# Kernel tuning notes

Measured on AMD Instinct MI355X. Metric: run time of the kernel, lower is better.

## Reference

```python
import jax, jax.numpy as jnp
import numpy as np
import math

B, SEQ_LEN, ENC_IN = 8, 1021, 12
D_MODEL, N_HEADS, D_FF, E_LAYERS = 512, 8, 2048, 3
FACTOR, NUM_CLASS = 5, 10
BN_EPS = 1e-5


def _pos_encoding(L, d):
    pos = np.arange(L, dtype=np.float32)[:, None]
    div = np.exp(np.arange(0, d, 2, dtype=np.float32) * (-math.log(10000.0) / d))
    pe = np.zeros((L, d), dtype=np.float32)
    pe[:, 0::2] = np.sin(pos * div)
    pe[:, 1::2] = np.cos(pos * div)
    return jnp.asarray(pe)


def _layer_norm(x, w, b, eps=1e-5):
    mu = jnp.mean(x, -1, keepdims=True)
    var = jnp.mean((x - mu) ** 2, -1, keepdims=True)
    return (x - mu) * jax.lax.rsqrt(var + eps) * w + b


def _circ_conv1d(x, w, b=None):
    # x: [B,C,L], w: [O,C,3]; circular pad 1 each side then valid conv (torch padding_mode='circular')
    xp = jnp.concatenate([x[..., -1:], x, x[..., :1]], axis=-1)
    y = jax.lax.conv_general_dilated(xp, w, (1,), 'VALID', dimension_numbers=('NCH', 'OIH', 'NCH'))
    return y if b is None else y + b[None, :, None]


def _prob_attention(q, k, v, rng):
    # ProbSparse attention (mask_flag=False). q,k,v: [B,H,L,Dh]
    Bq, H, L, Dh = q.shape
    n = min(FACTOR * int(math.ceil(math.log(L))), L)      # U_part == u (L_Q == L_K)
    idx = jax.random.randint(rng, (L, n), 0, L)           # sampled key ids per query
    k_sample = k[:, :, idx, :]                            # [B,H,L,n,Dh]
    qk_sample = jnp.einsum('bhld,bhlsd->bhls', q, k_sample)
    m = qk_sample.max(-1) - qk_sample.sum(-1) / L         # sparsity measure M
    _, m_top = jax.lax.top_k(m, n)                        # [B,H,n] active queries
    q_red = jnp.take_along_axis(q, m_top[..., None], axis=2)   # [B,H,n,Dh]
    scores = jnp.einsum('bhud,bhld->bhul', q_red, k) * (1.0 / math.sqrt(Dh))
    attn = jax.nn.softmax(scores, axis=-1)
    upd = jnp.einsum('bhul,bhld->bhud', attn, v)          # [B,H,n,Dh]
    ctx = jnp.broadcast_to(jnp.mean(v, axis=2, keepdims=True), (Bq, H, L, Dh))  # initial context = mean(V)
    b_ix = jnp.arange(Bq)[:, None, None]
    h_ix = jnp.arange(H)[None, :, None]
    ctx = ctx.at[b_ix, h_ix, m_top].set(upd)
    return jnp.transpose(ctx, (0, 2, 1, 3))               # [B,L,H,Dh]


def _encoder_layer(x, l, attn_wq, attn_bq, attn_wk, attn_bk, attn_wv, attn_bv,
                   attn_wo, attn_bo, ln1_w, ln1_b, ln2_w, ln2_b,
                   ff1_w, ff1_b, ff2_w, ff2_b, rng):
    Bx, L, dm = x.shape
    Dh = dm // N_HEADS
    q = (x @ attn_wq[l].T + attn_bq[l]).reshape(Bx, L, N_HEADS, Dh).transpose(0, 2, 1, 3)
    k = (x @ attn_wk[l].T + attn_bk[l]).reshape(Bx, L, N_HEADS, Dh).transpose(0, 2, 1, 3)
    v = (x @ attn_wv[l].T + attn_bv[l]).reshape(Bx, L, N_HEADS, Dh).transpose(0, 2, 1, 3)
    ctx = _prob_attention(q, k, v, rng).reshape(Bx, L, dm)
    new_x = ctx @ attn_wo[l].T + attn_bo[l]
    x = _layer_norm(x + new_x, ln1_w[l], ln1_b[l])
    y = jax.nn.gelu(x @ ff1_w[l].T + ff1_b[l], approximate=False)
    y = y @ ff2_w[l].T + ff2_b[l]
    return _layer_norm(x + y, ln2_w[l], ln2_b[l])


def _conv_layer(x, cw, cb, bnw, bnb):
    # distillation: circular conv -> BatchNorm (eval, mean 0 / var 1) -> ELU -> MaxPool(3,2,pad=1)
    h = _circ_conv1d(jnp.transpose(x, (0, 2, 1)), cw, cb)
    h = h * (bnw * (1.0 / math.sqrt(1.0 + BN_EPS)))[None, :, None] + bnb[None, :, None]
    h = jax.nn.elu(h)
    h = jax.lax.reduce_window(h, -np.inf, jax.lax.max, (1, 1, 3), (1, 1, 2),
                              ((0, 0), (0, 0), (1, 1)))
    return jnp.transpose(h, (0, 2, 1))


def _forward(x_enc, tok_w, attn_wq, attn_bq, attn_wk, attn_bk, attn_wv, attn_bv,
             attn_wo, attn_bo, ln1_w, ln1_b, ln2_w, ln2_b, ff1_w, ff1_b, ff2_w, ff2_b,
             cv_w, cv_b, bn_w, bn_b, norm_w, norm_b, proj_w, proj_b):
    rngs = jax.random.split(jax.random.key(42), E_LAYERS)
    # DataEmbedding = TokenEmbedding (circular conv, no bias) + sinusoidal positional
    x = jnp.transpose(_circ_conv1d(jnp.transpose(x_enc, (0, 2, 1)), tok_w), (0, 2, 1))
    x = x + _pos_encoding(x.shape[1], D_MODEL)[None]
    for l in range(E_LAYERS):
        x = _encoder_layer(x, l, attn_wq, attn_bq, attn_wk, attn_bk, attn_wv, attn_bv,
                           attn_wo, attn_bo, ln1_w, ln1_b, ln2_w, ln2_b,
                           ff1_w, ff1_b, ff2_w, ff2_b, rngs[l])
        if l < E_LAYERS - 1:
            x = _conv_layer(x, cv_w[l], cv_b[l], bn_w[l], bn_b[l])
    x = _layer_norm(x, norm_w, norm_b)
    out = jax.nn.gelu(x, approximate=False)
    out = out.reshape(out.shape[0], -1)    # [B, d_model * conv_seq_len]
    return out @ proj_w.T + proj_b


def setup_inputs() -> dict:
    key = jax.random.key(0)
    ks = jax.random.split(key, 32)
    d, ff = D_MODEL, D_FF

    def nrm(k, shape, scale=1.0):
        return jax.random.normal(k, shape, dtype=jnp.float32) * scale

    s_d = 1.0 / math.sqrt(d)
    return {
        'x_enc': nrm(ks[0], (B, SEQ_LEN, ENC_IN)),
        'tok_w': nrm(ks[1], (d, ENC_IN, 3), 1.0 / math.sqrt(ENC_IN * 3)),
        'attn_wq': nrm(ks[2], (E_LAYERS, d, d), s_d), 'attn_bq': nrm(ks[3], (E_LAYERS, d), 0.02),
        'attn_wk': nrm(ks[4], (E_LAYERS, d, d), s_d), 'attn_bk': nrm(ks[5], (E_LAYERS, d), 0.02),
        'attn_wv': nrm(ks[6], (E_LAYERS, d, d), s_d), 'attn_bv': nrm(ks[7], (E_LAYERS, d), 0.02),
        'attn_wo': nrm(ks[8], (E_LAYERS, d, d), s_d), 'attn_bo': nrm(ks[9], (E_LAYERS, d), 0.02),
        'ln1_w': jnp.ones((E_LAYERS, d), jnp.float32), 'ln1_b': jnp.zeros((E_LAYERS, d), jnp.float32),
        'ln2_w': jnp.ones((E_LAYERS, d), jnp.float32), 'ln2_b': jnp.zeros((E_LAYERS, d), jnp.float32),
        'ff1_w': nrm(ks[10], (E_LAYERS, ff, d), s_d), 'ff1_b': nrm(ks[11], (E_LAYERS, ff), 0.02),
        'ff2_w': nrm(ks[12], (E_LAYERS, d, ff), 1.0 / math.sqrt(ff)), 'ff2_b': nrm(ks[13], (E_LAYERS, d), 0.02),
        'cv_w': nrm(ks[14], (E_LAYERS - 1, d, d, 3), 1.0 / math.sqrt(3 * d)),
        'cv_b': nrm(ks[15], (E_LAYERS - 1, d), 0.02),
        'bn_w': jnp.ones((E_LAYERS - 1, d), jnp.float32), 'bn_b': jnp.zeros((E_LAYERS - 1, d), jnp.float32),
        'norm_w': jnp.ones((d,), jnp.float32), 'norm_b': jnp.zeros((d,), jnp.float32),
        'proj_w': nrm(ks[16], (NUM_CLASS, d * 256), 1.0 / math.sqrt(d * 256)),
        'proj_b': jnp.zeros((NUM_CLASS,), jnp.float32),
    }


def reference(x_enc, tok_w, attn_wq, attn_bq, attn_wk, attn_bk, attn_wv, attn_bv,
              attn_wo, attn_bo, ln1_w, ln1_b, ln2_w, ln2_b, ff1_w, ff1_b, ff2_w, ff2_b,
              cv_w, cv_b, bn_w, bn_b, norm_w, norm_b, proj_w, proj_b):
    return _forward(x_enc, tok_w, attn_wq, attn_bq, attn_wk, attn_bk, attn_wv, attn_bv,
                    attn_wo, attn_bo, ln1_w, ln1_b, ln2_w, ln2_b, ff1_w, ff1_b, ff2_w, ff2_b,
                    cv_w, cv_b, bn_w, bn_b, norm_w, norm_b, proj_w, proj_b)
```

## Files before the change

### kernel.cpp

```cpp
#include <hip/hip_runtime.h>
#include <math.h>
#include <stdint.h>

typedef __attribute__((ext_vector_type(8))) short bf16x8;
typedef __attribute__((ext_vector_type(4))) float f32x4;

__device__ __forceinline__ unsigned short f2bf(float f){
  unsigned int u = __float_as_uint(f);
  unsigned int r = (u + 0x7fffu + ((u>>16)&1u)) >> 16;
  return (unsigned short)r;
}
__device__ __forceinline__ float bf2f(unsigned short h){
  return __uint_as_float(((unsigned int)h)<<16);
}
__device__ __forceinline__ void gload16(const void* g, void* l){
  __builtin_amdgcn_global_load_lds(
      (const __attribute__((address_space(1))) unsigned int*)g,
      (__attribute__((address_space(3))) unsigned int*)l, 16, 0, 0);
}

__host__ __device__ static inline uint32_t rotl32(uint32_t x, int d){ return (x<<d)|(x>>(32-d)); }
__host__ __device__ static inline void tf2x32(uint32_t k0, uint32_t k1, uint32_t c0, uint32_t c1,
                                              uint32_t* o0, uint32_t* o1){
  uint32_t ks0=k0, ks1=k1, ks2=k0^k1^0x1BD11BDAu;
  uint32_t x0=c0+ks0, x1=c1+ks1;
  const int ra[4]={13,15,26,6}, rb[4]={17,29,16,24};
  #pragma unroll
  for(int i=0;i<4;i++){x0+=x1;x1=rotl32(x1,ra[i]);x1^=x0;}
  x0+=ks1; x1+=ks2+1u;
  #pragma unroll
  for(int i=0;i<4;i++){x0+=x1;x1=rotl32(x1,rb[i]);x1^=x0;}
  x0+=ks2; x1+=ks0+2u;
  #pragma unroll
  for(int i=0;i<4;i++){x0+=x1;x1=rotl32(x1,ra[i]);x1^=x0;}
  x0+=ks0; x1+=ks1+3u;
  #pragma unroll
  for(int i=0;i<4;i++){x0+=x1;x1=rotl32(x1,rb[i]);x1^=x0;}
  x0+=ks1; x1+=ks2+4u;
  #pragma unroll
  for(int i=0;i<4;i++){x0+=x1;x1=rotl32(x1,ra[i]);x1^=x0;}
  x0+=ks2; x1+=ks0+5u;
  *o0=x0; *o1=x1;
}

__global__ __launch_bounds__(256) void gen_idx_k(uint32_t k1a,uint32_t k1b,
                                                 uint32_t k2a,uint32_t k2b,
                                                 int size,uint32_t span,uint32_t mult,
                                                 int* __restrict__ idx){
  int i = blockIdx.x*256 + threadIdx.x;
  if (i >= size) return;
  uint32_t h0,h1,l0,l1;
  tf2x32(k1a,k1b,0u,(uint32_t)i,&h0,&h1);
  tf2x32(k2a,k2b,0u,(uint32_t)i,&l0,&l1);
  uint32_t hb = h0^h1, lb = l0^l1;
  idx[i] = (int)((((hb%span)*mult) + (lb%span)) % span);
}

__global__ __launch_bounds__(256) void embed_k(const float* __restrict__ xe,
                                               const float* __restrict__ tw,
                                               float* __restrict__ X,
                                               short* __restrict__ Xh){
  int i = blockIdx.x*256 + threadIdx.x;
  int c = i & 511;
  int bl = i >> 9;
  int l = bl % 1021;
  int b = bl / 1021;
  float acc = 0.f;
  #pragma unroll
  for (int t=0;t<3;t++){
    int ls = l - 1 + t;
    ls = (ls < 0) ? 1020 : (ls >= 1021 ? 0 : ls);
    const float* xp = xe + (size_t)(b*1021 + ls)*12;
    const float* wp = tw + (size_t)c*36 + t;
    #pragma unroll
    for (int ci=0; ci<12; ci++) acc += xp[ci] * wp[ci*3];
  }
  int ip = c >> 1;
  float div = expf((float)(2*ip) * (float)(-9.210340371976184/512.0));
  float ang = (float)l * div;
  acc += (c & 1) ? cosf(ang) : sinf(ang);
  X[i] = acc;
  Xh[i] = f2bf(acc);
}

__global__ __launch_bounds__(256) void wcvt_k(const float* __restrict__ src,
                                              short* __restrict__ dst, int n){
  int i = blockIdx.x*256 + threadIdx.x;
  if (i < n) dst[i] = f2bf(src[i]);
}
__global__ __launch_bounds__(256) void convw_k(const float* __restrict__ cw,
                                               short* __restrict__ W){
  int i = blockIdx.x*256 + threadIdx.x;
  int col = i % 1536; int co = i / 1536;
  int t = col / 512; int ci = col % 512;
  W[i] = f2bf(cw[(size_t)co*1536 + ci*3 + t]);
}

__global__ __launch_bounds__(256) void gemm_bf16_k(
    const short* __restrict__ A, long Ab,
    const short* __restrict__ W, long Wb,
    const float* __restrict__ bias,
    float* __restrict__ Cf, short* __restrict__ Ch, long Cb,
    int M, int Nreal, int Nstride, int K, int mode,
    const float* __restrict__ s2, const float* __restrict__ b2,
    const float* __restrict__ rs, long rsb,
    short* __restrict__ KhG, int Lq)
{
  __shared__ short As[8192];
  __shared__ short Bs[8192];
  const int t = threadIdx.x;
  const int lane = t & 63;
  const int w = t >> 6;
  const int wr = w >> 1, wc = w & 1;
  const int z = blockIdx.z;
  const int m0 = blockIdx.x * 128, n0 = blockIdx.y * 128;
  const short* Az = A + (size_t)z * Ab;
  const short* Wz = W + (size_t)z * Wb;

  f32x4 acc[4][4];
  #pragma unroll
  for (int i=0;i<4;i++)
    #pragma unroll
    for (int j=0;j<4;j++) acc[i][j] = (f32x4){0.f,0.f,0.f,0.f};

  const int r0  = t >> 2;
  const int k80 = (t & 3) << 3;
  char* AsB = (char*)As;
  char* BsB = (char*)Bs;

  #define STAGE(buf, k0) do { \
    gload16(Az + (size_t)(m0 + r0)      * K + (k0) + k80, AsB + (buf)*8192 + (size_t)w*1024); \
    gload16(Az + (size_t)(m0 + r0 + 64) * K + (k0) + k80, AsB + (buf)*8192 + 4096 + (size_t)w*1024); \
    gload16(Wz + (size_t)(n0 + r0)      * K + (k0) + k80, BsB + (buf)*8192 + (size_t)w*1024); \
    gload16(Wz + (size_t)(n0 + r0 + 64) * K + (k0) + k80, BsB + (buf)*8192 + 4096 + (size_t)w*1024); \
  } while(0)

  STAGE(0, 0);
  __syncthreads();
  int cur = 0;
  for (int k0 = 0; k0 < K; k0 += 32){
    if (k0 + 32 < K) STAGE(cur^1, k0+32);
    bf16x8 a[4], b[4];
    #pragma unroll
    for (int mi=0; mi<4; mi++){
      int aoff = cur*4096 + (wr*64 + mi*16 + (lane&15))*32 + ((lane>>4)<<3);
      a[mi] = *(const bf16x8*)(&As[aoff]);
    }
    #pragma unroll
    for (int ni=0; ni<4; ni++){
      int boff = cur*4096 + (wc*64 + ni*16 + (lane&15))*32 + ((lane>>4)<<3);
      b[ni] = *(const bf16x8*)(&Bs[boff]);
    }
    #pragma unroll
    for (int mi=0; mi<4; mi++)
      #pragma unroll
      for (int ni=0; ni<4; ni++)
        acc[mi][ni] = __builtin_amdgcn_mfma_f32_16x16x32_bf16(a[mi], b[ni], acc[mi][ni], 0, 0, 0);
    __syncthreads();
    cur ^= 1;
  }
  #undef STAGE

  #pragma unroll
  for (int mi=0; mi<4; mi++){
    #pragma unroll
    for (int r=0; r<4; r++){
      int gm = m0 + wr*64 + mi*16 + ((lane>>4)<<2) + r;
      if (gm >= M) continue;
      float rsc = (mode==4) ? rs[(size_t)z*rsb + gm] : 0.f;
      int bb = 0, ll = 0;
      if (KhG){ bb = gm / Lq; ll = gm - bb*Lq; }
      #pragma unroll
      for (int ni=0; ni<4; ni++){
        int gn = n0 + wc*64 + ni*16 + (lane&15);
        if (gn >= Nreal) continue;
        float v = acc[mi][ni][r];
        if (mode <= 2) v += bias[gn];
        if (mode == 1){
          v = 0.5f*v*(1.0f + erff(v*0.707106781186547524f));
        } else if (mode == 2){
          v = v * (s2[gn]*0.9999950000374997f) + b2[gn];
          v = (v > 0.f) ? v : expm1f(v);
        } else if (mode == 4){
          v *= rsc;
        }
        size_t off = (size_t)z*Cb + (size_t)gm*Nstride + gn;
        if (Cf) Cf[off] = v;
        if (Ch) Ch[off] = f2bf(v);
        if (KhG) KhG[(((size_t)bb*8 + (gn>>6))*1024 + ll)*64 + (gn&63)] = f2bf(v);
      }
    }
  }
}

__global__ __launch_bounds__(320) void qk_dot_k(const float* __restrict__ Q,
                                                const float* __restrict__ Kb,
                                                const int* __restrict__ idx,
                                                float* __restrict__ QK, int L, int n){
  __shared__ float Qs[512];
  int blk = blockIdx.x;
  int l = blk % L, b = blk / L;
  int t = threadIdx.x;
  if (t < 128){
    gload16(Q + (size_t)(b*L + l)*512 + t*4, (char*)Qs + (size_t)(t>>6)*1024);
  }
  __syncthreads();
  if (t < 8*n){
    int h = t / n, s = t - h*n;
    int kr = idx[l*n + s];
    const float4* kp = (const float4*)(Kb + (size_t)(b*L + kr)*512 + h*64);
    const float4* qp = (const float4*)(Qs + h*64);
    float dot = 0.f;
    #pragma unroll
    for (int i=0;i<16;i++){
      float4 a = qp[i], c = kp[i];
      dot += a.x*c.x + a.y*c.y + a.z*c.z + a.w*c.w;
    }
    QK[((size_t)(b*8 + h)*L + l)*n + s] = dot;
  }
}

__global__ __launch_bounds__(256) void reduce_m_k(const float* __restrict__ QK,
                                                  float* __restrict__ Mout, int L, int n){
  int gi = blockIdx.x*256 + threadIdx.x;
  if (gi >= 64*L) return;
  int l = gi % L; int bh = gi / L;
  const float* row = QK + (size_t)gi*n;
  float mx = -INFINITY, sm = 0.f;
  for (int s=0;s<n;s++){ float v = row[s]; mx = fmaxf(mx, v); sm += v; }
  Mout[(size_t)bh*1024 + l] = mx - sm/(float)L;
}

__global__ __launch_bounds__(64) void topk_k(const float* __restrict__ Mv,
                                             int* __restrict__ topk, int L, int n){
  int bh = blockIdx.x; int lane = threadIdx.x;
  float v[16];
  #pragma unroll
  for (int i=0;i<16;i++){ int l = i*64 + lane; v[i] = (l<L) ? Mv[(size_t)bh*1024 + l] : -INFINITY; }
  for (int it=0; it<n; ++it){
    float bv = -INFINITY; int bi = 0x7fffffff;
    #pragma unroll
    for (int i=0;i<16;i++){ int l = i*64+lane; if (v[i] > bv){ bv = v[i]; bi = l; } }
    #pragma unroll
    for (int o=32;o>0;o>>=1){
      float ov = __shfl_xor(bv, o); int oi = __shfl_xor(bi, o);
      if (ov > bv || (ov == bv && oi < bi)){ bv = ov; bi = oi; }
    }
    if (lane == 0) topk[bh*n + it] = bi;
    int wl = bi & 63, wi = bi >> 6;
    if (lane == wl){
      #pragma unroll
      for (int i=0;i<16;i++) if (i == wi) v[i] = -INFINITY;
    }
  }
}

__global__ __launch_bounds__(64) void qred_k(const float* __restrict__ Q,
                                             const int* __restrict__ topk,
                                             short* __restrict__ Qrh, int L, int n){
  int u = blockIdx.x % n; int bh = blockIdx.x / n;
  int h = bh & 7, b = bh >> 3; int d = threadIdx.x;
  int lq = topk[bh*n + u];
  Qrh[(size_t)bh*8192 + u*64 + d] = f2bf(0.125f * Q[(size_t)(b*L + lq)*512 + h*64 + d]);
}

__global__ __launch_bounds__(256) void vt_k(const float* __restrict__ V,
                                            short* __restrict__ Vt, int L){
  __shared__ float ts[64][65];
  int z = blockIdx.x >> 4;
  int l0 = (blockIdx.x & 15) * 64;
  int h = z & 7, b = z >> 3;
  int t = threadIdx.x;
  for (int i = t; i < 4096; i += 256){
    int lloc = i >> 6, d = i & 63;
    int l = l0 + lloc;
    ts[d][lloc] = (l < L) ? V[(size_t)(b*L + l)*512 + h*64 + d] : 0.f;
  }
  __syncthreads();
  for (int i = t; i < 4096; i += 256){
    int d = i >> 6, lloc = i & 63;
    Vt[(size_t)z*131072 + (size_t)d*1024 + l0 + lloc] = f2bf(ts[d][lloc]);
  }
}

__global__ __launch_bounds__(256) void softmax_k(const float* __restrict__ S,
                                                 short* __restrict__ Ph,
                                                 float* __restrict__ RS, int L, int n){
  int u = blockIdx.x % n; int z = blockIdx.x / n;
  const float* srow = S + (size_t)z*n*1024 + (size_t)u*1024;
  short* prow = Ph + (size_t)z*131072 + (size_t)u*1024;
  int t = threadIdx.x;
  __shared__ float red[256];
  float lm = -INFINITY;
  for (int l=t; l<L; l+=256) lm = fmaxf(lm, srow[l]);
  red[t]=lm; __syncthreads();
  for (int o=128;o>0;o>>=1){ if(t<o) red[t]=fmaxf(red[t],red[t+o]); __syncthreads(); }
  float mx = red[0]; __syncthreads();
  float ls = 0.f;
  for (int l=t; l<1024; l+=256){
    float p = (l < L) ? expf(srow[l]-mx) : 0.f;
    prow[l] = f2bf(p);
    ls += p;
  }
  red[t]=ls; __syncthreads();
  for (int o=128;o>0;o>>=1){ if(t<o) red[t]+=red[t+o]; __syncthreads(); }
  if (t==0) RS[(size_t)z*n + u] = 1.0f/red[0];
}

__global__ __launch_bounds__(512) void vmean_part_k(const float* __restrict__ V,
                                                    float* __restrict__ part, int L){
  int b = blockIdx.x; int j = blockIdx.y; int c = threadIdx.x;
  float s = 0.f;
  for (int l = j; l < L; l += 16) s += V[(size_t)(b*L + l)*512 + c];
  part[(size_t)(b*16 + j)*512 + c] = s;
}
__global__ __launch_bounds__(256) void vmean_comb_k(const float* __restrict__ part,
                                                    float* __restrict__ vmean, int L){
  int i = blockIdx.x*256 + threadIdx.x;
  int b = i >> 9; int c = i & 511;
  float s = 0.f;
  #pragma unroll
  for (int j=0;j<16;j++) s += part[(size_t)(b*16 + j)*512 + c];
  vmean[i] = s / (float)L;
}
__global__ __launch_bounds__(256) void ctx_fill_k(short* __restrict__ CTXh,
                                                  const float* __restrict__ vmean, int L){
  int i = blockIdx.x*256 + threadIdx.x;
  int c = i & 511; int bl = i >> 9; int b = bl / L;
  CTXh[i] = f2bf(vmean[b*512 + c]);
}
__global__ __launch_bounds__(256) void ctx_scatter_k(short* __restrict__ CTXh,
                                                     const float* __restrict__ UPD,
                                                     const int* __restrict__ topk, int L, int n){
  int i = blockIdx.x*256 + threadIdx.x;
  int d = i & 63; int u = (i >> 6) % n; int bh = i / (64*n);
  int h = bh & 7; int b = bh >> 3;
  int lq = topk[bh*n + u];
  CTXh[(size_t)(b*L + lq)*512 + h*64 + d] = f2bf(UPD[((size_t)bh*n + u)*64 + d]);
}

__global__ __launch_bounds__(256) void add_ln_k(float* __restrict__ X,
                                                short* __restrict__ Xh,
                                                const float* __restrict__ Y,
                                                const float* __restrict__ w,
                                                const float* __restrict__ b){
  int r = blockIdx.x;
  size_t base = (size_t)r*512;
  int t = threadIdx.x;
  float v0 = X[base+t]     + Y[base+t];
  float v1 = X[base+t+256] + Y[base+t+256];
  __shared__ float red[256];
  red[t] = v0 + v1; __syncthreads();
  for (int o=128;o>0;o>>=1){ if(t<o) red[t]+=red[t+o]; __syncthreads(); }
  float mu = red[0]*(1.f/512.f); __syncthreads();
  float d0 = v0-mu, d1 = v1-mu;
  red[t] = d0*d0 + d1*d1; __syncthreads();
  for (int o=128;o>0;o>>=1){ if(t<o) red[t]+=red[t+o]; __syncthreads(); }
  float rs = 1.0f/sqrtf(red[0]*(1.f/512.f) + 1e-5f);
  float x0 = d0*rs*w[t]     + b[t];
  float x1 = d1*rs*w[t+256] + b[t+256];
  X[base+t]     = x0;  Xh[base+t]     = f2bf(x0);
  X[base+t+256] = x1;  Xh[base+t+256] = f2bf(x1);
}

__global__ __launch_bounds__(256) void ln_gelu_k(const float* __restrict__ X,
                                                 float* __restrict__ Yout,
                                                 const float* __restrict__ w,
                                                 const float* __restrict__ b){
  int r = blockIdx.x;
  size_t base = (size_t)r*512;
  int t = threadIdx.x;
  float v0 = X[base+t];
  float v1 = X[base+t+256];
  __shared__ float red[256];
  red[t] = v0 + v1; __syncthreads();
  for (int o=128;o>0;o>>=1){ if(t<o) red[t]+=red[t+o]; __syncthreads(); }
  float mu = red[0]*(1.f/512.f); __syncthreads();
  float d0 = v0-mu, d1 = v1-mu;
  red[t] = d0*d0 + d1*d1; __syncthreads();
  for (int o=128;o>0;o>>=1){ if(t<o) red[t]+=red[t+o]; __syncthreads(); }
  float rs = 1.0f/sqrtf(red[0]*(1.f/512.f) + 1e-5f);
  float g0 = d0*rs*w[t]     + b[t];
  float g1 = d1*rs*w[t+256] + b[t+256];
  Yout[base+t]     = 0.5f*g0*(1.0f + erff(g0*0.707106781186547524f));
  Yout[base+t+256] = 0.5f*g1*(1.0f + erff(g1*0.707106781186547524f));
}

__global__ __launch_bounds__(256) void im2col_k(const float* __restrict__ X,
                                                short* __restrict__ O, int L){
  int i = blockIdx.x*256 + threadIdx.x;
  int col = i % 1536; int bl = i / 1536;
  int l = bl % L; int b = bl / L;
  int t = col / 512; int ci = col % 512;
  int ls = l - 1 + t;
  ls = (ls < 0) ? (L-1) : (ls >= L ? 0 : ls);
  O[(size_t)bl*1536 + col] = f2bf(X[(size_t)(b*L + ls)*512 + ci]);
}
__global__ __launch_bounds__(256) void pool_k(const short* __restrict__ Hc,
                                              float* __restrict__ X,
                                              short* __restrict__ Xh, int L, int Lo){
  int i = blockIdx.x*256 + threadIdx.x;
  int c = i & 511; int r = i >> 9; int lo = r % Lo; int b = r / Lo;
  float m = -INFINITY;
  #pragma unroll
  for (int dt=-1; dt<=1; dt++){
    int li = 2*lo + dt;
    if (li >= 0 && li < L) m = fmaxf(m, bf2f((unsigned short)Hc[(size_t)(b*L + li)*512 + c]));
  }
  size_t o = (size_t)(b*Lo + lo)*512 + c;
  X[o] = m; Xh[o] = f2bf(m);
}

__global__ __launch_bounds__(256) void proj_part_k(const float* __restrict__ Xg,
                                                   const float* __restrict__ pw,
                                                   float* __restrict__ part){
  int b = blockIdx.x >> 5;
  int c = blockIdx.x & 31;
  int t = threadIdx.x;
  const float4* xp = (const float4*)(Xg + (size_t)b*131072 + (size_t)c*4096);
  float4 x0 = xp[t], x1 = xp[t+256], x2 = xp[t+512], x3 = xp[t+768];
  float acc[10];
  #pragma unroll
  for (int j=0;j<10;j++){
    const float4* wp = (const float4*)(pw + (size_t)j*131072 + (size_t)c*4096);
    float4 w0 = wp[t], w1 = wp[t+256], w2 = wp[t+512], w3 = wp[t+768];
    acc[j] = x0.x*w0.x + x0.y*w0.y + x0.z*w0.z + x0.w*w0.w
           + x1.x*w1.x + x1.y*w1.y + x1.z*w1.z + x1.w*w1.w
           + x2.x*w2.x + x2.y*w2.y + x2.z*w2.z + x2.w*w2.w
           + x3.x*w3.x + x3.y*w3.y + x3.z*w3.z + x3.w*w3.w;
  }
  __shared__ float red[256];
  #pragma unroll
  for (int j=0;j<10;j++){
    red[t] = acc[j]; __syncthreads();
    for (int o=128;o>0;o>>=1){ if(t<o) red[t]+=red[t+o]; __syncthreads(); }
    if (t==0) part[(b*10 + j)*32 + c] = red[0];
    __syncthreads();
  }
}
__global__ __launch_bounds__(128) void proj_comb_k(const float* __restrict__ part,
                                                   const float* __restrict__ pb,
                                                   float* __restrict__ out){
  int t = threadIdx.x;
  if (t >= 80) return;
  int j = t % 10;
  const float* p = part + t*32;
  float s = 0.f;
  #pragma unroll
  for (int c=0;c<32;c++) s += p[c];
  out[t] = s + pb[j];
}

extern "C" void kernel_launch(void* const* d_in, const int* in_sizes, int n_in,
                              void* d_out, int out_size, void* d_ws, size_t ws_size,
                              hipStream_t stream){
  (void)in_sizes; (void)n_in; (void)out_size; (void)ws_size;
  const float* x_enc = (const float*)d_in[0];
  const float* tok_w = (const float*)d_in[1];
  const float* wq    = (const float*)d_in[2];
  const float* bq    = (const float*)d_in[3];
  const float* wk    = (const float*)d_in[4];
  const float* bk    = (const float*)d_in[5];
  const float* wvp   = (const float*)d_in[6];
  const float* bvp   = (const float*)d_in[7];
  const float* wo    = (const float*)d_in[8];
  const float* bo    = (const float*)d_in[9];
  const float* ln1w  = (const float*)d_in[10];
  const float* ln1b  = (const float*)d_in[11];
  const float* ln2w  = (const float*)d_in[12];
  const float* ln2b  = (const float*)d_in[13];
  const float* f1w   = (const float*)d_in[14];
  const float* f1b   = (const float*)d_in[15];
  const float* f2w   = (const float*)d_in[16];
  const float* f2b   = (const float*)d_in[17];
  const float* cvw   = (const float*)d_in[18];
  const float* cvb   = (const float*)d_in[19];
  const float* bnw   = (const float*)d_in[20];
  const float* bnb   = (const float*)d_in[21];
  const float* nw    = (const float*)d_in[22];
  const float* nb    = (const float*)d_in[23];
  const float* pw    = (const float*)d_in[24];
  const float* pb    = (const float*)d_in[25];

  char* wsb = (char*)d_ws;
  float* X    = (float*)(wsb + 0);
  float* Y    = (float*)(wsb + 16777216);
  float* Q    = (float*)(wsb + 33554432);
  float* Kbuf = (float*)(wsb + 50331648);
  float* V    = (float*)(wsb + 67108864);
  short* Xh   = (short*)(wsb + 83886080);
  short* CTXh = (short*)(wsb + 92274688);
  short* WQH  = (short*)(wsb + 100663296);
  short* WKH  = WQH + 262144;
  short* WVH  = WKH + 262144;
  short* WOH  = WVH + 262144;
  short* F1H  = WOH + 262144;
  short* F2H  = F1H + 1048576;
  short* WCVH = F2H + 1048576;
  char*  RB   = wsb + 108527616;
  short* FFh  = (short*)(RB);
  short* IM2  = (short*)(RB + 33554432);
  short* Kh   = (short*)(RB + 0);
  short* Vt   = (short*)(RB + 8388608);
  short* Ph   = (short*)(RB + 25165824);
  short* Qrh  = (short*)(RB + 41943040);
  float* S    = (float*)(RB + 42991616);
  float* RS   = (float*)(RB + 52166656);
  float* UPD  = (float*)(RB + 52175616);
  float* Mb   = (float*)(RB + 52749056);
  float* VME  = (float*)(RB + 53011200);
  float* VPA  = (float*)(RB + 53027584);
  int*   IDX  = (int*)  (RB + 53289728);
  int*   TOPK = (int*)  (RB + 53433088);
  float* PPART= (float*)(RB + 53450752);

  uint32_t rka[3], rkb[3];
  for (int l = 0; l < 3; ++l) tf2x32(0u, 42u, 0u, (uint32_t)l, &rka[l], &rkb[l]);

  auto gemm = [&](const short* A, long Ab, const short* W, long Wb, const float* bias,
                  float* Cf, short* Ch, long Cb, int M, int Nreal, int Nstride, int K,
                  int mode, const float* s2, const float* b2, const float* rs, long rsb,
                  int mt, int nt, int zt, short* KhG, int Lq){
    hipLaunchKernelGGL(gemm_bf16_k, dim3(mt, nt, zt), dim3(256), 0, stream,
                       A, Ab, W, Wb, bias, Cf, Ch, Cb, M, Nreal, Nstride, K, mode,
                       s2, b2, rs, rsb, KhG, Lq);
  };

  hipLaunchKernelGGL(embed_k, dim3(16336), dim3(256), 0, stream, x_enc, tok_w, X, Xh);

  int L = 1021;
  for (int l = 0; l < 3; ++l){
    int n = 5 * (int)ceil(log((double)L)); if (n > L) n = L;
    int Mr = 8 * L;
    int mt = (Mr + 127)/128;

    hipLaunchKernelGGL(wcvt_k, dim3(1024), dim3(256), 0, stream, wq + (size_t)l*262144, WQH, 262144);
    hipLaunchKernelGGL(wcvt_k, dim3(1024), dim3(256), 0, stream, wk + (size_t)l*262144, WKH, 262144);
    hipLaunchKernelGGL(wcvt_k, dim3(1024), dim3(256), 0, stream, wvp+ (size_t)l*262144, WVH, 262144);
    hipLaunchKernelGGL(wcvt_k, dim3(1024), dim3(256), 0, stream, wo + (size_t)l*262144, WOH, 262144);
    hipLaunchKernelGGL(wcvt_k, dim3(4096), dim3(256), 0, stream, f1w+ (size_t)l*1048576, F1H, 1048576);
    hipLaunchKernelGGL(wcvt_k, dim3(4096), dim3(256), 0, stream, f2w+ (size_t)l*1048576, F2H, 1048576);

    uint32_t k1a,k1b,k2a,k2b;
    tf2x32(rka[l], rkb[l], 0u, 0u, &k1a, &k1b);
    tf2x32(rka[l], rkb[l], 0u, 1u, &k2a, &k2b);
    int size = L * n;
    uint32_t span = (uint32_t)L;
    uint32_t rr = 65536u % span;
    uint32_t mult = (rr * rr) % span;
    hipLaunchKernelGGL(gen_idx_k, dim3((unsigned)((size+255)/256)), dim3(256), 0, stream,
                       k1a, k1b, k2a, k2b, size, span, mult, IDX);

    gemm(Xh, 0, WQH, 0, bq + (size_t)l*512, Q,    nullptr, 0, Mr, 512, 512, 512, 0, 0, 0, 0, 0, mt, 4, 1, nullptr, 0);
    gemm(Xh, 0, WKH, 0, bk + (size_t)l*512, Kbuf, nullptr, 0, Mr, 512, 512, 512, 0, 0, 0, 0, 0, mt, 4, 1, Kh, L);
    gemm(Xh, 0, WVH, 0, bvp+ (size_t)l*512, V,    nullptr, 0, Mr, 512, 512, 512, 0, 0, 0, 0, 0, mt, 4, 1, nullptr, 0);

    hipLaunchKernelGGL(qk_dot_k, dim3((unsigned)(8*L)), dim3(320), 0, stream,
                       Q, Kbuf, IDX, S, L, n);
    hipLaunchKernelGGL(reduce_m_k, dim3((unsigned)((64*L+255)/256)), dim3(256), 0, stream,
                       S, Mb, L, n);
    hipLaunchKernelGGL(topk_k, dim3(64), dim3(64), 0, stream, Mb, TOPK, L, n);

    hipLaunchKernelGGL(qred_k, dim3((unsigned)(64*n)), dim3(64), 0, stream, Q, TOPK, Qrh, L, n);
    hipLaunchKernelGGL(vt_k, dim3(1024), dim3(256), 0, stream, V, Vt, L);
    gemm(Qrh, 8192, Kh, 65536, nullptr, S, nullptr, (long)n*1024, n, L, 1024, 64, 3, 0, 0, 0, 0, 1, 8, 64, nullptr, 0);
    hipLaunchKernelGGL(softmax_k, dim3((unsigned)(64*n)), dim3(256), 0, stream, S, Ph, RS, L, n);
    gemm(Ph, 131072, Vt, 131072, nullptr, UPD, nullptr, (long)n*64, n, 64, 64, 1024, 4, 0, 0, RS, n, 1, 1, 64, nullptr, 0);

    hipLaunchKernelGGL(vmean_part_k, dim3(8,16), dim3(512), 0, stream, V, VPA, L);
    hipLaunchKernelGGL(vmean_comb_k, dim3(16), dim3(256), 0, stream, VPA, VME, L);
    hipLaunchKernelGGL(ctx_fill_k, dim3((unsigned)(Mr*2)), dim3(256), 0, stream, CTXh, VME, L);
    hipLaunchKernelGGL(ctx_scatter_k, dim3((unsigned)(16*n)), dim3(256), 0, stream, CTXh, UPD, TOPK, L, n);

    gemm(CTXh, 0, WOH, 0, bo + (size_t)l*512, Y, nullptr, 0, Mr, 512, 512, 512, 0, 0, 0, 0, 0, mt, 4, 1, nullptr, 0);
    hipLaunchKernelGGL(add_ln_k, dim3((unsigned)Mr), dim3(256), 0, stream, X, Xh, Y, ln1w + (size_t)l*512, ln1b + (size_t)l*512);

    gemm(Xh, 0, F1H, 0, f1b + (size_t)l*2048, nullptr, FFh, 0, Mr, 2048, 2048, 512, 1, 0, 0, 0, 0, mt, 16, 1, nullptr, 0);
    gemm(FFh, 0, F2H, 0, f2b + (size_t)l*512, Y, nullptr, 0, Mr, 512, 512, 2048, 0, 0, 0, 0, 0, mt, 4, 1, nullptr, 0);
    hipLaunchKernelGGL(add_ln_k, dim3((unsigned)Mr), dim3(256), 0, stream, X, Xh, Y, ln2w + (size_t)l*512, ln2b + (size_t)l*512);

    if (l < 2){
      hipLaunchKernelGGL(convw_k, dim3(3072), dim3(256), 0, stream, cvw + (size_t)l*786432, WCVH);
      hipLaunchKernelGGL(im2col_k, dim3((unsigned)(Mr*6)), dim3(256), 0, stream, X, IM2, L);
      gemm(IM2, 0, WCVH, 0, cvb + (size_t)l*512, nullptr, CTXh, 0, Mr, 512, 512, 1536, 2,
           bnw + (size_t)l*512, bnb + (size_t)l*512, 0, 0, mt, 4, 1, nullptr, 0);
      int Lo = (L - 1)/2 + 1;
      hipLaunchKernelGGL(pool_k, dim3((unsigned)(8*Lo*2)), dim3(256), 0, stream, CTXh, X, Xh, L, Lo);
      L = Lo;
    }
  }

  hipLaunchKernelGGL(ln_gelu_k, dim3((unsigned)(8*L)), dim3(256), 0, stream, X, Y, nw, nb);
  hipLaunchKernelGGL(proj_part_k, dim3(256), dim3(256), 0, stream, Y, pw, PPART);
  hipLaunchKernelGGL(proj_comb_k, dim3(1), dim3(128), 0, stream, PPART, pb, (float*)d_out);
}
```

Baseline: 1.685 ms.

## Fuse sampled QK dot products with sparsity-measure reduction and coalesce key loads

The sampled Q·K dot-product kernel now computes the per-query max-minus-mean sparsity measure itself, keeping the dots in shared memory. This removes the separate reduction kernel and the global round-trip of the QK sample buffer. Key loads are restructured so each wavefront reads a full 512-float key row in a coalesced way, reducing per head with lane shuffles instead of one thread per (head, sample) reading 64 floats serially. The shared dots array is sized for n up to 36, which the L=1021 case (n=35) fits.

```diff
diff --git a/kernel.cpp b/kernel.cpp
--- a/kernel.cpp
+++ b/kernel.cpp
@@ -193,42 +193,39 @@
   }
 }
 
-__global__ __launch_bounds__(320) void qk_dot_k(const float* __restrict__ Q,
+__global__ __launch_bounds__(256) void qk_dot_k(const float* __restrict__ Q,
                                                 const float* __restrict__ Kb,
                                                 const int* __restrict__ idx,
-                                                float* __restrict__ QK, int L, int n){
+                                                float* __restrict__ Mout, int L, int n){
   __shared__ float Qs[512];
+  __shared__ float dots[8][36];
   int blk = blockIdx.x;
   int l = blk % L, b = blk / L;
   int t = threadIdx.x;
+  int w = t >> 6, lane = t & 63;
   if (t < 128){
     gload16(Q + (size_t)(b*L + l)*512 + t*4, (char*)Qs + (size_t)(t>>6)*1024);
   }
   __syncthreads();
-  if (t < 8*n){
-    int h = t / n, s = t - h*n;
+  const float4* qp = (const float4*)(Qs + lane*8);
+  float4 q0 = qp[0], q1 = qp[1];
+  for (int s = w; s < n; s += 4){
     int kr = idx[l*n + s];
-    const float4* kp = (const float4*)(Kb + (size_t)(b*L + kr)*512 + h*64);
-    const float4* qp = (const float4*)(Qs + h*64);
-    float dot = 0.f;
-    #pragma unroll
-    for (int i=0;i<16;i++){
-      float4 a = qp[i], c = kp[i];
-      dot += a.x*c.x + a.y*c.y + a.z*c.z + a.w*c.w;
-    }
-    QK[((size_t)(b*8 + h)*L + l)*n + s] = dot;
-  }
-}
-
-__global__ __launch_bounds__(256) void reduce_m_k(const float* __restrict__ QK,
-                                                  float* __restrict__ Mout, int L, int n){
-  int gi = blockIdx.x*256 + threadIdx.x;
-  if (gi >= 64*L) return;
-  int l = gi % L; int bh = gi / L;
-  const float* row = QK + (size_t)gi*n;
-  float mx = -INFINITY, sm = 0.f;
-  for (int s=0;s<n;s++){ float v = row[s]; mx = fmaxf(mx, v); sm += v; }
-  Mout[(size_t)bh*1024 + l] = mx - sm/(float)L;
+    const float4* kp = (const float4*)(Kb + (size_t)(b*L + kr)*512 + lane*8);
+    float4 a0 = kp[0], a1 = kp[1];
+    float p = a0.x*q0.x + a0.y*q0.y + a0.z*q0.z + a0.w*q0.w
+            + a1.x*q1.x + a1.y*q1.y + a1.z*q1.z + a1.w*q1.w;
+    p += __shfl_xor(p, 1);
+    p += __shfl_xor(p, 2);
+    p += __shfl_xor(p, 4);
+    if ((lane & 7) == 0) dots[lane >> 3][s] = p;
+  }
+  __syncthreads();
+  if (t < 8){
+    float mx = -INFINITY, sm = 0.f;
+    for (int s = 0; s < n; ++s){ float v = dots[t][s]; mx = fmaxf(mx, v); sm += v; }
+    Mout[(size_t)(b*8 + t)*1024 + l] = mx - sm/(float)L;
+  }
 }
 
 __global__ __launch_bounds__(64) void topk_k(const float* __restrict__ Mv,
@@ -555,10 +552,8 @@
     gemm(Xh, 0, WKH, 0, bk + (size_t)l*512, Kbuf, nullptr, 0, Mr, 512, 512, 512, 0, 0, 0, 0, 0, mt, 4, 1, Kh, L);
     gemm(Xh, 0, WVH, 0, bvp+ (size_t)l*512, V,    nullptr, 0, Mr, 512, 512, 512, 0, 0, 0, 0, 0, mt, 4, 1, nullptr, 0);
 
-    hipLaunchKernelGGL(qk_dot_k, dim3((unsigned)(8*L)), dim3(320), 0, stream,
-                       Q, Kbuf, IDX, S, L, n);
-    hipLaunchKernelGGL(reduce_m_k, dim3((unsigned)((64*L+255)/256)), dim3(256), 0, stream,
-                       S, Mb, L, n);
+    hipLaunchKernelGGL(qk_dot_k, dim3((unsigned)(8*L)), dim3(256), 0, stream,
+                       Q, Kbuf, IDX, Mb, L, n);
     hipLaunchKernelGGL(topk_k, dim3(64), dim3(64), 0, stream, Mb, TOPK, L, n);
 
     hipLaunchKernelGGL(qred_k, dim3((unsigned)(64*n)), dim3(64), 0, stream, Q, TOPK, Qrh, L, n);
```

Measured after the change: 1.567 ms. -7.0%, faster.
